# Kernel tuning notes

Hardware: AMD Instinct MI355X
Metric: run time of the kernel (lower is better)

Reference implementation:

```python
import jax, jax.numpy as jnp
import numpy as np


def setup_inputs() -> dict:
    key = jax.random.key(0)
    k1, k2 = jax.random.split(key)
    B, S, D = 64, 1024, 768
    batch = jax.random.normal(k1, (B, S, D), dtype=jnp.float32)
    # nn.init.uniform_(proj, -0.05, 0.05)
    proj = jax.random.uniform(k2, (D, D), minval=-0.05, maxval=0.05, dtype=jnp.float32)
    return {"batch": batch, "proj": proj}


def reference(batch, proj):
    """dists[b,i,j] = (h_i - h_j)^T A (h_i - h_j)
    Expanded: h_i^T A h_i + h_j^T A h_j - h_i^T A h_j - h_j^T A h_i.
    Avoids the O(B*S^2*D) diffs tensor of the original.
    """
    # P[b,i,:] = h_i^T A  -> (B, S, D)
    P = jnp.einsum('bid,de->bie', batch, proj)
    # cross[b,i,j] = h_i^T A h_j -> (B, S, S)
    cross = jnp.einsum('bie,bje->bij', P, batch)
    q = jnp.einsum('bii->bi', cross)  # h_i^T A h_i, (B, S)
    dists = q[:, :, None] + q[:, None, :] - cross - jnp.swapaxes(cross, 1, 2)
    return dists
```

## Files before the change

kernel.cpp:

```cpp
#include <hip/hip_runtime.h>

#define GLOBAL_AS __attribute__((address_space(1)))
#define LDS_AS    __attribute__((address_space(3)))

typedef __bf16 bf16_t;
typedef __bf16 bf16x8 __attribute__((ext_vector_type(8)));
typedef __bf16 bf16x4 __attribute__((ext_vector_type(4)));
typedef float  f32x4  __attribute__((ext_vector_type(4)));

#define BATCH 64
#define SEQ   1024
#define DIM   768
#define BS_ROWS (BATCH * SEQ)

__device__ __forceinline__ void gl2lds16(const void* g, void* l) {
    __builtin_amdgcn_global_load_lds((GLOBAL_AS const void*)g, (LDS_AS void*)l, 16, 0, 0);
}

__global__ void k_zero(float* __restrict__ p, int n) {
    int gid = blockIdx.x * 256 + threadIdx.x;
    if (gid < n) p[gid] = 0.f;
}

__global__ void k_convert(const float* __restrict__ x, bf16_t* __restrict__ y, int n8) {
    int gid = blockIdx.x * 256 + threadIdx.x;
    if (gid >= n8) return;
    const float4* xp = (const float4*)x;
    float4 a = xp[gid * 2];
    float4 b = xp[gid * 2 + 1];
    bf16x8 v;
    v[0] = (bf16_t)a.x; v[1] = (bf16_t)a.y; v[2] = (bf16_t)a.z; v[3] = (bf16_t)a.w;
    v[4] = (bf16_t)b.x; v[5] = (bf16_t)b.y; v[6] = (bf16_t)b.z; v[7] = (bf16_t)b.w;
    ((bf16x8*)y)[gid] = v;
}

__global__ void k_asym(const float* __restrict__ A, bf16_t* __restrict__ S_, int n) {
    int idx = blockIdx.x * 256 + threadIdx.x;
    if (idx >= n) return;
    int d = idx / DIM;
    int e = idx - d * DIM;
    S_[idx] = (bf16_t)(A[idx] + A[e * DIM + d]);
}

__global__ void k_gemm1(const bf16_t* __restrict__ H, const bf16_t* __restrict__ Ag,
                        bf16_t* __restrict__ M, float* __restrict__ qv) {
    __shared__ bf16_t Asm[128 * 32];
    __shared__ bf16_t Bsm[128 * 32];
    const int t = threadIdx.x;
    const int g = blockIdx.x;
    const int tile = (g & 7) * 384 + (g >> 3);
    const int row0 = (tile / 6) * 128;
    const int col0 = (tile % 6) * 128;
    const int ln = t & 63, w = t >> 6;
    const int wr = w >> 1, wc = w & 1;
    const int r = ln & 15, qd = ln >> 4;
    const int sseg = qd ^ ((r >> 1) & 3);

    const int srow = t >> 2;
    const int gseg = (t & 3) ^ ((t >> 3) & 3);
    const bf16_t* gA0 = H  + (size_t)(row0 + srow) * DIM + gseg * 8;
    const bf16_t* gA1 = gA0 + (size_t)64 * DIM;
    const bf16_t* gB0 = Ag + (size_t)(col0 + srow) * DIM + gseg * 8;
    const bf16_t* gB1 = gB0 + (size_t)64 * DIM;

    f32x4 acc[4][4] = {};

    for (int k0 = 0; k0 < DIM; k0 += 32) {
        gl2lds16(gA0 + k0, &Asm[t * 8]);
        gl2lds16(gA1 + k0, &Asm[2048 + t * 8]);
        gl2lds16(gB0 + k0, &Bsm[t * 8]);
        gl2lds16(gB1 + k0, &Bsm[2048 + t * 8]);
        __syncthreads();

        bf16x8 af[4], bf[4];
#pragma unroll
        for (int mt = 0; mt < 4; ++mt) {
            int m = wr * 64 + mt * 16 + r;
            af[mt] = *(const bf16x8*)&Asm[m * 32 + sseg * 8];
        }
#pragma unroll
        for (int nt = 0; nt < 4; ++nt) {
            int n = wc * 64 + nt * 16 + r;
            bf[nt] = *(const bf16x8*)&Bsm[n * 32 + sseg * 8];
        }
#pragma unroll
        for (int mt = 0; mt < 4; ++mt)
#pragma unroll
            for (int nt = 0; nt < 4; ++nt)
                acc[mt][nt] = __builtin_amdgcn_mfma_f32_16x16x32_bf16(
                    af[mt], bf[nt], acc[mt][nt], 0, 0, 0);
        __syncthreads();
    }

#pragma unroll
    for (int mt = 0; mt < 4; ++mt) {
#pragma unroll
        for (int rI = 0; rI < 4; ++rI) {
            int row = row0 + wr * 64 + mt * 16 + qd * 4 + rI;
            size_t base = (size_t)row * DIM + col0 + wc * 64;
            float s = 0.f;
#pragma unroll
            for (int nt = 0; nt < 4; ++nt) {
                bf16_t mv = (bf16_t)acc[mt][nt][rI];
                M[base + nt * 16 + r] = mv;
                s += (float)mv * (float)H[base + nt * 16 + r];
            }
            s += __shfl_xor(s, 1, 64);
            s += __shfl_xor(s, 2, 64);
            s += __shfl_xor(s, 4, 64);
            s += __shfl_xor(s, 8, 64);
            if (r == 0) atomicAdd(&qv[row], 0.5f * s);
        }
    }
}

__global__ void k_gemm2(const bf16_t* __restrict__ M, const bf16_t* __restrict__ H,
                        const float* __restrict__ qv, float* __restrict__ out) {
    __shared__ __align__(16) char smem[16640];
    bf16_t* Asm = (bf16_t*)smem;
    bf16_t* Bsm = (bf16_t*)(smem + 8192);
    float*  Tsm = (float*)smem;

    const int t = threadIdx.x;
    const int g = blockIdx.x;
    const int u = (g & 7) * 288 + (g >> 3);
    const int b = u / 36;
    int l = u - b * 36;
    int ti = 0;
    while (l >= 8 - ti) { l -= 8 - ti; ++ti; }
    const int tj = ti + l;
    const int row0 = ti * 128;
    const int col0 = tj * 128;

    const int ln = t & 63, w = t >> 6;
    const int wr = w >> 1, wc = w & 1;
    const int r = ln & 15, qd = ln >> 4;
    const int sseg = qd ^ ((r >> 1) & 3);

    const bf16_t* Mb = M + (size_t)b * SEQ * DIM;
    const bf16_t* Hb = H + (size_t)b * SEQ * DIM;

    const int srow = t >> 2;
    const int gseg = (t & 3) ^ ((t >> 3) & 3);
    const bf16_t* gA0 = Mb + (size_t)(row0 + srow) * DIM + gseg * 8;
    const bf16_t* gA1 = gA0 + (size_t)64 * DIM;
    const bf16_t* gB0 = Hb + (size_t)(col0 + srow) * DIM + gseg * 8;
    const bf16_t* gB1 = gB0 + (size_t)64 * DIM;

    f32x4 acc[4][4] = {};

    for (int k0 = 0; k0 < DIM; k0 += 32) {
        gl2lds16(gA0 + k0, &Asm[t * 8]);
        gl2lds16(gA1 + k0, &Asm[2048 + t * 8]);
        gl2lds16(gB0 + k0, &Bsm[t * 8]);
        gl2lds16(gB1 + k0, &Bsm[2048 + t * 8]);
        __syncthreads();

        bf16x8 af[4], bf[4];
#pragma unroll
        for (int mt = 0; mt < 4; ++mt) {
            int m = wr * 64 + mt * 16 + r;
            af[mt] = *(const bf16x8*)&Asm[m * 32 + sseg * 8];
        }
#pragma unroll
        for (int nt = 0; nt < 4; ++nt) {
            int n = wc * 64 + nt * 16 + r;
            bf[nt] = *(const bf16x8*)&Bsm[n * 32 + sseg * 8];
        }
#pragma unroll
        for (int mt = 0; mt < 4; ++mt)
#pragma unroll
            for (int nt = 0; nt < 4; ++nt)
                acc[mt][nt] = __builtin_amdgcn_mfma_f32_16x16x32_bf16(
                    af[mt], bf[nt], acc[mt][nt], 0, 0, 0);
        __syncthreads();
    }

    const float* qb = qv + b * SEQ;
    float qc[4];
#pragma unroll
    for (int nt = 0; nt < 4; ++nt) qc[nt] = qb[col0 + wc * 64 + nt * 16 + r];

#pragma unroll
    for (int mt = 0; mt < 4; ++mt) {
#pragma unroll
        for (int rI = 0; rI < 4; ++rI) {
            int row = row0 + wr * 64 + mt * 16 + qd * 4 + rI;
            float qr = qb[row];
            size_t base = ((size_t)b * SEQ + row) * SEQ + col0 + wc * 64;
#pragma unroll
            for (int nt = 0; nt < 4; ++nt)
                out[base + nt * 16 + r] = qr + qc[nt] - acc[mt][nt][rI];
        }
    }

    if (ti != tj) {
#pragma unroll
        for (int c = 0; c < 4; ++c) {
            __syncthreads();
            if (wr == (c >> 1)) {
                const int m0 = (c & 1) * 2;
#pragma unroll
                for (int mi = 0; mi < 2; ++mi) {
                    const int mt = m0 + mi;
#pragma unroll
                    for (int rI = 0; rI < 4; ++rI) {
                        int lrow = mi * 16 + qd * 4 + rI;
                        int row = row0 + wr * 64 + mt * 16 + qd * 4 + rI;
                        float qr = qb[row];
#pragma unroll
                        for (int nt = 0; nt < 4; ++nt) {
                            int lcol = wc * 64 + nt * 16 + r;
                            Tsm[lrow * 130 + lcol] = qr + qc[nt] - acc[mt][nt][rI];
                        }
                    }
                }
            }
            __syncthreads();
            const int rowbase = row0 + 32 * c;
#pragma unroll
            for (int i = 0; i < 16; ++i) {
                int lin = i * 256 + t;
                int lrow = lin & 31;
                int lcol = lin >> 5;
                out[((size_t)b * SEQ + col0 + lcol) * SEQ + rowbase + lrow] =
                    Tsm[lrow * 130 + lcol];
            }
        }
    }
}

extern "C" void kernel_launch(void* const* d_in, const int* in_sizes, int n_in,
                              void* d_out, int out_size, void* d_ws, size_t ws_size,
                              hipStream_t stream) {
    const float* batch = (const float*)d_in[0];
    const float* proj  = (const float*)d_in[1];
    float* out = (float*)d_out;

    char* ws = (char*)d_ws;
    bf16_t* Hb = (bf16_t*)ws;
    bf16_t* Mb = (bf16_t*)(ws + 100663296);
    bf16_t* Ab = (bf16_t*)(ws + 201326592);
    float*  qv = (float*)(ws + 202506240);

    k_zero<<<256, 256, 0, stream>>>(qv, BS_ROWS);
    k_convert<<<24576, 256, 0, stream>>>(batch, Hb, 6291456);
    k_asym<<<2304, 256, 0, stream>>>(proj, Ab, DIM * DIM);
    k_gemm1<<<3072, 256, 0, stream>>>(Hb, Ab, Mb, qv);
    k_gemm2<<<2304, 256, 0, stream>>>(Mb, Hb, qv, out);
}
```

Baseline: 687.7 us.

## Move diagonal q computation into diagonal-tile GEMM and split gemm2 launches

Merges the convert and symmetrization kernels into one prep launch and drops the qv zeroing kernel. The q_i = 0.5*h_i^T(A+A^T)h_i reduction no longer uses atomics in the gemm1 epilogue. It is now computed inside a new diagonal-tile kernel from the M and H tiles already staged in LDS, and written to qv before the off-diagonal kernel reads it. This removes the atomics and extra H reads in gemm1, at the cost of an extra launch and a dependency ordering between the diagonal and off-diagonal kernels.

```diff
diff --git a/kernel.cpp b/kernel.cpp
--- a/kernel.cpp
+++ b/kernel.cpp
@@ -5,7 +5,6 @@
 
 typedef __bf16 bf16_t;
 typedef __bf16 bf16x8 __attribute__((ext_vector_type(8)));
-typedef __bf16 bf16x4 __attribute__((ext_vector_type(4)));
 typedef float  f32x4  __attribute__((ext_vector_type(4)));
 
 #define BATCH 64
@@ -17,33 +16,28 @@
     __builtin_amdgcn_global_load_lds((GLOBAL_AS const void*)g, (LDS_AS void*)l, 16, 0, 0);
 }
 
-__global__ void k_zero(float* __restrict__ p, int n) {
-    int gid = blockIdx.x * 256 + threadIdx.x;
-    if (gid < n) p[gid] = 0.f;
-}
-
-__global__ void k_convert(const float* __restrict__ x, bf16_t* __restrict__ y, int n8) {
-    int gid = blockIdx.x * 256 + threadIdx.x;
-    if (gid >= n8) return;
-    const float4* xp = (const float4*)x;
-    float4 a = xp[gid * 2];
-    float4 b = xp[gid * 2 + 1];
-    bf16x8 v;
-    v[0] = (bf16_t)a.x; v[1] = (bf16_t)a.y; v[2] = (bf16_t)a.z; v[3] = (bf16_t)a.w;
-    v[4] = (bf16_t)b.x; v[5] = (bf16_t)b.y; v[6] = (bf16_t)b.z; v[7] = (bf16_t)b.w;
-    ((bf16x8*)y)[gid] = v;
-}
-
-__global__ void k_asym(const float* __restrict__ A, bf16_t* __restrict__ S_, int n) {
-    int idx = blockIdx.x * 256 + threadIdx.x;
-    if (idx >= n) return;
-    int d = idx / DIM;
-    int e = idx - d * DIM;
-    S_[idx] = (bf16_t)(A[idx] + A[e * DIM + d]);
+__global__ void k_prep(const float* __restrict__ batch, const float* __restrict__ proj,
+                       bf16_t* __restrict__ Hb, bf16_t* __restrict__ Ab) {
+    int bid = blockIdx.x;
+    if (bid < 24576) {
+        int gid = bid * 256 + threadIdx.x;
+        const float4* xp = (const float4*)batch;
+        float4 a = xp[gid * 2];
+        float4 b = xp[gid * 2 + 1];
+        bf16x8 v;
+        v[0] = (bf16_t)a.x; v[1] = (bf16_t)a.y; v[2] = (bf16_t)a.z; v[3] = (bf16_t)a.w;
+        v[4] = (bf16_t)b.x; v[5] = (bf16_t)b.y; v[6] = (bf16_t)b.z; v[7] = (bf16_t)b.w;
+        ((bf16x8*)Hb)[gid] = v;
+    } else {
+        int idx = (bid - 24576) * 256 + threadIdx.x;
+        int d = idx / DIM;
+        int e = idx - d * DIM;
+        Ab[idx] = (bf16_t)(proj[idx] + proj[e * DIM + d]);
+    }
 }
 
 __global__ void k_gemm1(const bf16_t* __restrict__ H, const bf16_t* __restrict__ Ag,
-                        bf16_t* __restrict__ M, float* __restrict__ qv) {
+                        bf16_t* __restrict__ M) {
     __shared__ bf16_t Asm[128 * 32];
     __shared__ bf16_t Bsm[128 * 32];
     const int t = threadIdx.x;
@@ -98,23 +92,109 @@
         for (int rI = 0; rI < 4; ++rI) {
             int row = row0 + wr * 64 + mt * 16 + qd * 4 + rI;
             size_t base = (size_t)row * DIM + col0 + wc * 64;
-            float s = 0.f;
-#pragma unroll
-            for (int nt = 0; nt < 4; ++nt) {
-                bf16_t mv = (bf16_t)acc[mt][nt][rI];
-                M[base + nt * 16 + r] = mv;
-                s += (float)mv * (float)H[base + nt * 16 + r];
-            }
-            s += __shfl_xor(s, 1, 64);
-            s += __shfl_xor(s, 2, 64);
-            s += __shfl_xor(s, 4, 64);
-            s += __shfl_xor(s, 8, 64);
-            if (r == 0) atomicAdd(&qv[row], 0.5f * s);
-        }
-    }
-}
-
-__global__ void k_gemm2(const bf16_t* __restrict__ M, const bf16_t* __restrict__ H,
+#pragma unroll
+            for (int nt = 0; nt < 4; ++nt)
+                M[base + nt * 16 + r] = (bf16_t)acc[mt][nt][rI];
+        }
+    }
+}
+
+__global__ void k_g2diag(const bf16_t* __restrict__ M, const bf16_t* __restrict__ H,
+                         float* __restrict__ qv, float* __restrict__ out) {
+    __shared__ bf16_t Asm[128 * 32];
+    __shared__ bf16_t Bsm[128 * 32];
+    __shared__ float qsm[128];
+    const int t = threadIdx.x;
+    const int g = blockIdx.x;
+    const int u = (g & 7) * 64 + (g >> 3);
+    const int b = u >> 3;
+    const int ti = u & 7;
+    const int row0 = ti * 128;
+
+    const int ln = t & 63, w = t >> 6;
+    const int wr = w >> 1, wc = w & 1;
+    const int r = ln & 15, qd = ln >> 4;
+    const int sseg = qd ^ ((r >> 1) & 3);
+
+    const bf16_t* Mb = M + (size_t)b * SEQ * DIM;
+    const bf16_t* Hb = H + (size_t)b * SEQ * DIM;
+
+    const int srow = t >> 2;
+    const int gseg = (t & 3) ^ ((t >> 3) & 3);
+    const bf16_t* gA0 = Mb + (size_t)(row0 + srow) * DIM + gseg * 8;
+    const bf16_t* gA1 = gA0 + (size_t)64 * DIM;
+    const bf16_t* gB0 = Hb + (size_t)(row0 + srow) * DIM + gseg * 8;
+    const bf16_t* gB1 = gB0 + (size_t)64 * DIM;
+
+    f32x4 acc[4][4] = {};
+    float s0 = 0.f, s1 = 0.f;
+
+    for (int k0 = 0; k0 < DIM; k0 += 32) {
+        gl2lds16(gA0 + k0, &Asm[t * 8]);
+        gl2lds16(gA1 + k0, &Asm[2048 + t * 8]);
+        gl2lds16(gB0 + k0, &Bsm[t * 8]);
+        gl2lds16(gB1 + k0, &Bsm[2048 + t * 8]);
+        __syncthreads();
+
+        bf16x8 va0 = *(const bf16x8*)&Asm[t * 8];
+        bf16x8 vb0 = *(const bf16x8*)&Bsm[t * 8];
+        bf16x8 va1 = *(const bf16x8*)&Asm[2048 + t * 8];
+        bf16x8 vb1 = *(const bf16x8*)&Bsm[2048 + t * 8];
+#pragma unroll
+        for (int j = 0; j < 8; ++j) {
+            s0 += (float)va0[j] * (float)vb0[j];
+            s1 += (float)va1[j] * (float)vb1[j];
+        }
+
+        bf16x8 af[4], bfv[4];
+#pragma unroll
+        for (int mt = 0; mt < 4; ++mt) {
+            int m = wr * 64 + mt * 16 + r;
+            af[mt] = *(const bf16x8*)&Asm[m * 32 + sseg * 8];
+        }
+#pragma unroll
+        for (int nt = 0; nt < 4; ++nt) {
+            int n = wc * 64 + nt * 16 + r;
+            bfv[nt] = *(const bf16x8*)&Bsm[n * 32 + sseg * 8];
+        }
+#pragma unroll
+        for (int mt = 0; mt < 4; ++mt)
+#pragma unroll
+            for (int nt = 0; nt < 4; ++nt)
+                acc[mt][nt] = __builtin_amdgcn_mfma_f32_16x16x32_bf16(
+                    af[mt], bfv[nt], acc[mt][nt], 0, 0, 0);
+        __syncthreads();
+    }
+
+    s0 += __shfl_xor(s0, 1, 64); s0 += __shfl_xor(s0, 2, 64);
+    s1 += __shfl_xor(s1, 1, 64); s1 += __shfl_xor(s1, 2, 64);
+    if ((t & 3) == 0) {
+        float q0 = 0.5f * s0, q1 = 0.5f * s1;
+        qsm[srow] = q0; qsm[64 + srow] = q1;
+        qv[(size_t)b * SEQ + row0 + srow] = q0;
+        qv[(size_t)b * SEQ + row0 + 64 + srow] = q1;
+    }
+    __syncthreads();
+
+    float qc[4];
+#pragma unroll
+    for (int nt = 0; nt < 4; ++nt) qc[nt] = qsm[wc * 64 + nt * 16 + r];
+
+#pragma unroll
+    for (int mt = 0; mt < 4; ++mt) {
+#pragma unroll
+        for (int rI = 0; rI < 4; ++rI) {
+            int lrow = wr * 64 + mt * 16 + qd * 4 + rI;
+            float qr = qsm[lrow];
+            size_t base = ((size_t)b * SEQ + row0 + lrow) * SEQ + row0 + wc * 64;
+#pragma unroll
+            for (int nt = 0; nt < 4; ++nt)
+                out[base + nt * 16 + r] = qr + qc[nt] - acc[mt][nt][rI];
+        }
+    }
+}
+
+__global__ void k_g2off(const bf16_t* __restrict__ M, const bf16_t* __restrict__ H,
                         const float* __restrict__ qv, float* __restrict__ out) {
     __shared__ __align__(16) char smem[16640];
     bf16_t* Asm = (bf16_t*)smem;
@@ -123,12 +203,12 @@
 
     const int t = threadIdx.x;
     const int g = blockIdx.x;
-    const int u = (g & 7) * 288 + (g >> 3);
-    const int b = u / 36;
-    int l = u - b * 36;
+    const int u = (g & 7) * 224 + (g >> 3);
+    const int b = u / 28;
+    int l = u - b * 28;
     int ti = 0;
-    while (l >= 8 - ti) { l -= 8 - ti; ++ti; }
-    const int tj = ti + l;
+    while (l >= 7 - ti) { l -= 7 - ti; ++ti; }
+    const int tj = ti + 1 + l;
     const int row0 = ti * 128;
     const int col0 = tj * 128;
 
@@ -156,7 +236,7 @@
         gl2lds16(gB1 + k0, &Bsm[2048 + t * 8]);
         __syncthreads();
 
-        bf16x8 af[4], bf[4];
+        bf16x8 af[4], bfv[4];
 #pragma unroll
         for (int mt = 0; mt < 4; ++mt) {
             int m = wr * 64 + mt * 16 + r;
@@ -165,18 +245,18 @@
 #pragma unroll
         for (int nt = 0; nt < 4; ++nt) {
             int n = wc * 64 + nt * 16 + r;
-            bf[nt] = *(const bf16x8*)&Bsm[n * 32 + sseg * 8];
+            bfv[nt] = *(const bf16x8*)&Bsm[n * 32 + sseg * 8];
         }
 #pragma unroll
         for (int mt = 0; mt < 4; ++mt)
 #pragma unroll
             for (int nt = 0; nt < 4; ++nt)
                 acc[mt][nt] = __builtin_amdgcn_mfma_f32_16x16x32_bf16(
-                    af[mt], bf[nt], acc[mt][nt], 0, 0, 0);
-        __syncthreads();
-    }
-
-    const float* qb = qv + b * SEQ;
+                    af[mt], bfv[nt], acc[mt][nt], 0, 0, 0);
+        __syncthreads();
+    }
+
+    const float* qb = qv + (size_t)b * SEQ;
     float qc[4];
 #pragma unroll
     for (int nt = 0; nt < 4; ++nt) qc[nt] = qb[col0 + wc * 64 + nt * 16 + r];
@@ -194,38 +274,36 @@
         }
     }
 
-    if (ti != tj) {
-#pragma unroll
-        for (int c = 0; c < 4; ++c) {
-            __syncthreads();
-            if (wr == (c >> 1)) {
-                const int m0 = (c & 1) * 2;
-#pragma unroll
-                for (int mi = 0; mi < 2; ++mi) {
-                    const int mt = m0 + mi;
-#pragma unroll
-                    for (int rI = 0; rI < 4; ++rI) {
-                        int lrow = mi * 16 + qd * 4 + rI;
-                        int row = row0 + wr * 64 + mt * 16 + qd * 4 + rI;
-                        float qr = qb[row];
-#pragma unroll
-                        for (int nt = 0; nt < 4; ++nt) {
-                            int lcol = wc * 64 + nt * 16 + r;
-                            Tsm[lrow * 130 + lcol] = qr + qc[nt] - acc[mt][nt][rI];
-                        }
+#pragma unroll
+    for (int c = 0; c < 4; ++c) {
+        __syncthreads();
+        if (wr == (c >> 1)) {
+            const int m0 = (c & 1) * 2;
+#pragma unroll
+            for (int mi = 0; mi < 2; ++mi) {
+                const int mt = m0 + mi;
+#pragma unroll
+                for (int rI = 0; rI < 4; ++rI) {
+                    int lrow = mi * 16 + qd * 4 + rI;
+                    int row = row0 + wr * 64 + mt * 16 + qd * 4 + rI;
+                    float qr = qb[row];
+#pragma unroll
+                    for (int nt = 0; nt < 4; ++nt) {
+                        int lcol = wc * 64 + nt * 16 + r;
+                        Tsm[lrow * 130 + lcol] = qr + qc[nt] - acc[mt][nt][rI];
                     }
                 }
             }
-            __syncthreads();
-            const int rowbase = row0 + 32 * c;
-#pragma unroll
-            for (int i = 0; i < 16; ++i) {
-                int lin = i * 256 + t;
-                int lrow = lin & 31;
-                int lcol = lin >> 5;
-                out[((size_t)b * SEQ + col0 + lcol) * SEQ + rowbase + lrow] =
-                    Tsm[lrow * 130 + lcol];
-            }
+        }
+        __syncthreads();
+        const int rowbase = row0 + 32 * c;
+#pragma unroll
+        for (int i = 0; i < 16; ++i) {
+            int lin = i * 256 + t;
+            int lrow = lin & 31;
+            int lcol = lin >> 5;
+            out[((size_t)b * SEQ + col0 + lcol) * SEQ + rowbase + lrow] =
+                Tsm[lrow * 130 + lcol];
         }
     }
 }
@@ -243,9 +321,8 @@
     bf16_t* Ab = (bf16_t*)(ws + 201326592);
     float*  qv = (float*)(ws + 202506240);
 
-    k_zero<<<256, 256, 0, stream>>>(qv, BS_ROWS);
-    k_convert<<<24576, 256, 0, stream>>>(batch, Hb, 6291456);
-    k_asym<<<2304, 256, 0, stream>>>(proj, Ab, DIM * DIM);
-    k_gemm1<<<3072, 256, 0, stream>>>(Hb, Ab, Mb, qv);
-    k_gemm2<<<2304, 256, 0, stream>>>(Mb, Hb, qv, out);
-}
+    k_prep<<<26880, 256, 0, stream>>>(batch, proj, Hb, Ab);
+    k_gemm1<<<3072, 256, 0, stream>>>(Hb, Ab, Mb);
+    k_g2diag<<<512, 256, 0, stream>>>(Mb, Hb, qv, out);
+    k_g2off<<<1792, 256, 0, stream>>>(Mb, Hb, qv, out);
+}
```

Result: faster. 637.7 us (-7.3%).
